# Kernel tuning notes

Measured on AMD Instinct MI355X. Metric: run time of the kernel, lower is better.

Reference implementation:

```python
import jax, jax.numpy as jnp
import numpy as np

N_NODES = 100000
N_EDGES = 3200000
F_IN = 256
CH = 16
FCN = 64


def setup_inputs() -> dict:
    key = jax.random.key(0)
    ks = jax.random.split(key, 8)
    x = jax.random.normal(ks[0], (N_NODES, F_IN), dtype=jnp.float32)
    edge_index = jax.random.randint(ks[1], (2, N_EDGES), 0, N_NODES, dtype=jnp.int64)
    edge_w = jax.random.uniform(ks[2], (N_EDGES,), dtype=jnp.float32)
    w_gcn = jax.random.normal(ks[3], (F_IN, CH), dtype=jnp.float32) * (1.0 / np.sqrt(F_IN))
    w0 = jax.random.normal(ks[4], (CH, FCN), dtype=jnp.float32) * (1.0 / np.sqrt(CH))
    b0 = jnp.zeros((FCN,), dtype=jnp.float32)
    w1 = jax.random.normal(ks[5], (FCN, 1), dtype=jnp.float32) * (1.0 / np.sqrt(FCN))
    b1 = jnp.zeros((1,), dtype=jnp.float32)
    return {"x": x, "edge_index": edge_index, "edge_w": edge_w,
            "w_gcn": w_gcn, "w0": w0, "b0": b0, "w1": w1, "b1": b1}


def reference(x, edge_index, edge_w, w_gcn, b0, b1, w0, w1):
    # GCNConv (Spektral): out = relu(A_norm @ (X @ W)); A_norm given as weighted edge list.
    # Dropout layers are identity at inference.
    src = edge_index[0]
    dst = edge_index[1]
    h = x @ w_gcn                                   # [N, CH] feature transform
    msgs = h[src] * edge_w[:, None]                 # [E, CH] gather + scale (irregular access)
    agg = jax.ops.segment_sum(msgs, dst, num_segments=N_NODES)  # [N, CH] scatter-add
    gcn_out = jax.nn.relu(agg)
    # Flatten on [N, CH] is identity (N acts as batch); per-node FCN head.
    o1 = jax.nn.relu(gcn_out @ w0 + b0)             # [N, FCN]
    o2 = o1 @ w1 + b1                               # [N, 1]
    return o2
```

## Files before the change

### kernel.cpp

```cpp
#include <hip/hip_runtime.h>

#define N_NODES 100000
#define N_EDGES 3200000
#define F_IN 256
#define CH 16
#define FCN 64

#define NPB 64
#define NBUCK 1563
#define NCHUNK 1024
#define EPB (N_EDGES / NCHUNK)
#define M (NBUCK * NCHUNK)
#define NSB (M / 1024)
#define ACCP 17
#define CAP 2560

__device__ __forceinline__ unsigned short f2bf(float f) {
    unsigned u = __float_as_uint(f);
    unsigned r = (u + 0x7FFFu + ((u >> 16) & 1u)) >> 16;
    return (unsigned short)r;
}

__global__ __launch_bounds__(256) void k_transform(const float* __restrict__ x,
                                                   const float* __restrict__ w,
                                                   unsigned short* __restrict__ h) {
    __shared__ float wlds[CH][F_IN + 4];
    int tid = threadIdx.x;
    for (int i = tid; i < F_IN * CH; i += 256) {
        int k = i >> 4, c = i & 15;
        wlds[c][k] = w[i];
    }
    __syncthreads();
    int c = tid & 15;
    int r = tid >> 4;
    int row = blockIdx.x * 16 + r;
    if (row >= N_NODES) return;
    const float4* xr = reinterpret_cast<const float4*>(x + (size_t)row * F_IN);
    const float4* wr = reinterpret_cast<const float4*>(&wlds[c][0]);
    float acc = 0.f;
    #pragma unroll 8
    for (int k4 = 0; k4 < F_IN / 4; ++k4) {
        float4 xv = xr[k4];
        float4 wv = wr[k4];
        acc = fmaf(xv.x, wv.x, acc);
        acc = fmaf(xv.y, wv.y, acc);
        acc = fmaf(xv.z, wv.z, acc);
        acc = fmaf(xv.w, wv.w, acc);
    }
    h[(size_t)row * CH + c] = f2bf(acc);
}

__global__ __launch_bounds__(256) void k_hist_rank(const int* __restrict__ ei,
                                                   unsigned short* __restrict__ rank16,
                                                   int* __restrict__ histM) {
    __shared__ int hist[NBUCK];
    int t = threadIdx.x, k = blockIdx.x;
    for (int i = t; i < NBUCK; i += 256) hist[i] = 0;
    __syncthreads();
    int base = k * EPB;
    for (int i = t; i < EPB; i += 256) {
        int e = base + i;
        int dst = ei[N_EDGES + e];
        int r = atomicAdd(&hist[dst >> 6], 1);
        rank16[e] = (unsigned short)r;
    }
    __syncthreads();
    for (int i = t; i < NBUCK; i += 256) histM[(size_t)i * NCHUNK + k] = hist[i];
}

__global__ __launch_bounds__(256) void k_scanP1(const int* __restrict__ histM,
                                                int* __restrict__ partials) {
    __shared__ int wsum[4];
    int t = threadIdx.x;
    int4 v = reinterpret_cast<const int4*>(histM)[blockIdx.x * 256 + t];
    int s = v.x + v.y + v.z + v.w;
    #pragma unroll
    for (int off = 32; off > 0; off >>= 1) s += __shfl_xor(s, off, 64);
    if ((t & 63) == 0) wsum[t >> 6] = s;
    __syncthreads();
    if (t == 0) partials[blockIdx.x] = wsum[0] + wsum[1] + wsum[2] + wsum[3];
}

__global__ __launch_bounds__(1024) void k_scanP2(const int* __restrict__ partials,
                                                 int* __restrict__ bases) {
    __shared__ int wsum[16];
    int t = threadIdx.x;
    int i0 = 2 * t, i1 = 2 * t + 1;
    int a = (i0 < NSB) ? partials[i0] : 0;
    int b = (i1 < NSB) ? partials[i1] : 0;
    int s = a + b;
    int lane = t & 63, w = t >> 6;
    int incl = s;
    #pragma unroll
    for (int off = 1; off < 64; off <<= 1) {
        int u = __shfl_up(incl, off, 64);
        if (lane >= off) incl += u;
    }
    if (lane == 63) wsum[w] = incl;
    __syncthreads();
    if (t == 0) {
        int run = 0;
        #pragma unroll
        for (int i = 0; i < 16; ++i) { int u = wsum[i]; wsum[i] = run; run += u; }
    }
    __syncthreads();
    int excl = incl - s + wsum[w];
    if (i0 <= NSB) bases[i0] = excl;
    if (i1 <= NSB) bases[i1] = excl + a;
}

__global__ __launch_bounds__(256) void k_scanP3(const int* __restrict__ histM,
                                                const int* __restrict__ bases,
                                                int* __restrict__ offs2d) {
    __shared__ int wsum[4];
    int t = threadIdx.x;
    int gi = blockIdx.x * 256 + t;
    int4 v = reinterpret_cast<const int4*>(histM)[gi];
    int s = v.x + v.y + v.z + v.w;
    int lane = t & 63, w = t >> 6;
    int incl = s;
    #pragma unroll
    for (int off = 1; off < 64; off <<= 1) {
        int u = __shfl_up(incl, off, 64);
        if (lane >= off) incl += u;
    }
    if (lane == 63) wsum[w] = incl;
    __syncthreads();
    if (t == 0) {
        int a = wsum[0], b = wsum[1], c = wsum[2];
        wsum[0] = 0; wsum[1] = a; wsum[2] = a + b; wsum[3] = a + b + c;
    }
    __syncthreads();
    int excl = incl - s + wsum[w] + bases[blockIdx.x];
    int4 o;
    o.x = excl;
    o.y = excl + v.x;
    o.z = o.y + v.y;
    o.w = o.z + v.z;
    reinterpret_cast<int4*>(offs2d)[gi] = o;
    if (blockIdx.x == 0 && t == 0) offs2d[M] = bases[NSB];
}

__global__ __launch_bounds__(256) void k_scatter2(const int* __restrict__ ei,
                                                  const float* __restrict__ ew,
                                                  const unsigned short* __restrict__ rank16,
                                                  const int* __restrict__ offs2d,
                                                  int2* __restrict__ recs) {
    __shared__ int coffs[NBUCK];
    int t = threadIdx.x, k = blockIdx.x;
    for (int i = t; i < NBUCK; i += 256) coffs[i] = offs2d[(size_t)i * NCHUNK + k];
    __syncthreads();
    int base = k * EPB;
    for (int i = t; i < EPB; i += 256) {
        int e = base + i;
        int src = ei[e];
        int dst = ei[N_EDGES + e];
        int b = dst >> 6;
        int local = dst & (NPB - 1);
        int pos = coffs[b] + (int)rank16[e];
        int2 r;
        r.x = src | (local << 17);
        r.y = __float_as_int(ew[e]);
        recs[pos] = r;
    }
}

__global__ __launch_bounds__(256) void k_agg_head(const int2* __restrict__ recs,
                                                  const int* __restrict__ offs2d,
                                                  const unsigned short* __restrict__ h,
                                                  const float* __restrict__ w0,
                                                  const float* __restrict__ b0,
                                                  const float* __restrict__ w1,
                                                  const float* __restrict__ b1,
                                                  float* __restrict__ out) {
    __shared__ int2 sorted[CAP];
    __shared__ float acc[NPB * ACCP];
    __shared__ float w0s[CH * FCN];
    __shared__ float w1s[FCN];
    __shared__ int hist64[NPB];
    __shared__ int base64[NPB];
    __shared__ int cur64[NPB];
    int t = threadIdx.x;
    int b = blockIdx.x;
    for (int i = t; i < NPB * ACCP; i += 256) acc[i] = 0.f;
    for (int i = t; i < CH * FCN; i += 256) w0s[i] = w0[i];
    if (t < FCN) w1s[t] = w1[t];
    if (t < NPB) hist64[t] = 0;
    __syncthreads();
    int start = offs2d[(size_t)b * NCHUNK];
    int end   = offs2d[(size_t)(b + 1) * NCHUNK];
    for (int j = start + t; j < end; j += 256) {
        int2 r = recs[j];
        atomicAdd(&hist64[r.x >> 17], 1);
    }
    __syncthreads();
    if (t < 64) {
        int v = hist64[t];
        int incl = v;
        #pragma unroll
        for (int off = 1; off < 64; off <<= 1) {
            int u = __shfl_up(incl, off, 64);
            if (t >= off) incl += u;
        }
        int excl = incl - v;
        base64[t] = excl;
        cur64[t] = excl;
    }
    __syncthreads();
    for (int j = start + t; j < end; j += 256) {
        int2 r = recs[j];
        int nl = r.x >> 17;
        int pos = atomicAdd(&cur64[nl], 1);
        if (pos < CAP) {
            sorted[pos] = r;
        } else {
            int src = r.x & 0x1FFFF;
            float wv = __int_as_float(r.y);
            const uint4* hp = reinterpret_cast<const uint4*>(h + (size_t)src * CH);
            uint4 ha = hp[0], hb = hp[1];
            float* a = &acc[nl * ACCP];
            unsafeAtomicAdd(a + 0,  __uint_as_float(ha.x << 16) * wv);
            unsafeAtomicAdd(a + 1,  __uint_as_float(ha.x & 0xFFFF0000u) * wv);
            unsafeAtomicAdd(a + 2,  __uint_as_float(ha.y << 16) * wv);
            unsafeAtomicAdd(a + 3,  __uint_as_float(ha.y & 0xFFFF0000u) * wv);
            unsafeAtomicAdd(a + 4,  __uint_as_float(ha.z << 16) * wv);
            unsafeAtomicAdd(a + 5,  __uint_as_float(ha.z & 0xFFFF0000u) * wv);
            unsafeAtomicAdd(a + 6,  __uint_as_float(ha.w << 16) * wv);
            unsafeAtomicAdd(a + 7,  __uint_as_float(ha.w & 0xFFFF0000u) * wv);
            unsafeAtomicAdd(a + 8,  __uint_as_float(hb.x << 16) * wv);
            unsafeAtomicAdd(a + 9,  __uint_as_float(hb.x & 0xFFFF0000u) * wv);
            unsafeAtomicAdd(a + 10, __uint_as_float(hb.y << 16) * wv);
            unsafeAtomicAdd(a + 11, __uint_as_float(hb.y & 0xFFFF0000u) * wv);
            unsafeAtomicAdd(a + 12, __uint_as_float(hb.z << 16) * wv);
            unsafeAtomicAdd(a + 13, __uint_as_float(hb.z & 0xFFFF0000u) * wv);
            unsafeAtomicAdd(a + 14, __uint_as_float(hb.w << 16) * wv);
            unsafeAtomicAdd(a + 15, __uint_as_float(hb.w & 0xFFFF0000u) * wv);
        }
    }
    __syncthreads();
    int nl = t >> 2, q = t & 3;
    int kb = base64[nl];
    int ke = min(kb + hist64[nl], CAP);
    float a0 = 0.f, a1 = 0.f, a2 = 0.f, a3 = 0.f;
    for (int k = kb; k < ke; ++k) {
        int2 r = sorted[k];
        int src  = r.x & 0x1FFFF;
        float wv = __int_as_float(r.y);
        uint2 hv = reinterpret_cast<const uint2*>(h)[src * 4 + q];
        a0 = fmaf(__uint_as_float(hv.x << 16),         wv, a0);
        a1 = fmaf(__uint_as_float(hv.x & 0xFFFF0000u), wv, a1);
        a2 = fmaf(__uint_as_float(hv.y << 16),         wv, a2);
        a3 = fmaf(__uint_as_float(hv.y & 0xFFFF0000u), wv, a3);
    }
    float* ap = &acc[nl * ACCP + q * 4];
    ap[0] += a0; ap[1] += a1; ap[2] += a2; ap[3] += a3;
    __syncthreads();
    int lane = t & 63, wv4 = t >> 6;
    float bb = b0[lane];
    float w1l = w1s[lane];
    float bias1 = b1[0];
    for (int n2 = wv4 * 16; n2 < wv4 * 16 + 16; ++n2) {
        int node = b * NPB + n2;
        if (node >= N_NODES) break;
        float o1 = bb;
        #pragma unroll
        for (int kk = 0; kk < CH; ++kk) {
            float a = fmaxf(acc[n2 * ACCP + kk], 0.f);
            o1 = fmaf(a, w0s[kk * FCN + lane], o1);
        }
        o1 = fmaxf(o1, 0.f);
        float y = o1 * w1l;
        #pragma unroll
        for (int off = 32; off > 0; off >>= 1) y += __shfl_xor(y, off, 64);
        if (lane == 0) out[node] = y + bias1;
    }
}

__global__ __launch_bounds__(256) void k_scatter_fb(const int* __restrict__ ei,
                                                    const float* __restrict__ ew,
                                                    const unsigned short* __restrict__ h,
                                                    float* __restrict__ agg) {
    long long t = (long long)blockIdx.x * 256 + threadIdx.x;
    int e = (int)(t >> 2);
    int g = (int)(t & 3);
    if (e >= N_EDGES) return;
    int src = ei[e];
    int dst = ei[N_EDGES + e];
    float w = ew[e];
    uint2 hv = reinterpret_cast<const uint2*>(h)[src * 4 + g];
    float* ap = agg + (size_t)dst * CH + g * 4;
    atomicAdd(ap + 0, __uint_as_float(hv.x << 16) * w);
    atomicAdd(ap + 1, __uint_as_float(hv.x & 0xFFFF0000u) * w);
    atomicAdd(ap + 2, __uint_as_float(hv.y << 16) * w);
    atomicAdd(ap + 3, __uint_as_float(hv.y & 0xFFFF0000u) * w);
}

__global__ __launch_bounds__(256) void k_head_fb(const float* __restrict__ agg,
                                                 const float* __restrict__ w0,
                                                 const float* __restrict__ b0,
                                                 const float* __restrict__ w1,
                                                 const float* __restrict__ b1,
                                                 float* __restrict__ out) {
    __shared__ float w0s[CH * FCN];
    __shared__ float w1s[FCN];
    int tid = threadIdx.x;
    for (int i = tid; i < CH * FCN; i += 256) w0s[i] = w0[i];
    if (tid < FCN) w1s[tid] = w1[tid];
    __syncthreads();
    int lane = tid & 63;
    int wv = tid >> 6;
    int node = blockIdx.x * 4 + wv;
    if (node >= N_NODES) return;
    const float* an = agg + (size_t)node * CH;
    float o1 = b0[lane];
    #pragma unroll
    for (int k = 0; k < CH; ++k) {
        float a = fmaxf(an[k], 0.f);
        o1 = fmaf(a, w0s[k * FCN + lane], o1);
    }
    o1 = fmaxf(o1, 0.f);
    float y = o1 * w1s[lane];
    #pragma unroll
    for (int off = 32; off > 0; off >>= 1) y += __shfl_xor(y, off, 64);
    if (lane == 0) out[node] = y + b1[0];
}

extern "C" void kernel_launch(void* const* d_in, const int* in_sizes, int n_in,
                              void* d_out, int out_size, void* d_ws, size_t ws_size,
                              hipStream_t stream) {
    const float* x  = (const float*)d_in[0];
    const int*   ei = (const int*)  d_in[1];
    const float* ew = (const float*)d_in[2];
    const float* wg = (const float*)d_in[3];
    const float* w0 = (const float*)d_in[4];
    const float* b0 = (const float*)d_in[5];
    const float* w1 = (const float*)d_in[6];
    const float* b1 = (const float*)d_in[7];
    float* out = (float*)d_out;

    char* p = (char*)d_ws;
    unsigned short* h = (unsigned short*)p;      p += 3200000;
    unsigned short* rank16 = (unsigned short*)p; p += 6400000;
    int* histM = (int*)p;                        p += (size_t)M * 4;
    int* offs2d = (int*)p;                       p += 6402304;
    int* partials = (int*)p;                     p += 6400;
    int* bases = (int*)p;                        p += 6400;
    int2* recs = (int2*)p;                       p += (size_t)N_EDGES * 8;
    const size_t need = (size_t)(p - (char*)d_ws);

    if (ws_size >= need) {
        k_transform<<<(N_NODES + 15) / 16, 256, 0, stream>>>(x, wg, h);
        k_hist_rank<<<NCHUNK, 256, 0, stream>>>(ei, rank16, histM);
        k_scanP1<<<NSB, 256, 0, stream>>>(histM, partials);
        k_scanP2<<<1, 1024, 0, stream>>>(partials, bases);
        k_scanP3<<<NSB, 256, 0, stream>>>(histM, bases, offs2d);
        k_scatter2<<<NCHUNK, 256, 0, stream>>>(ei, ew, rank16, offs2d, recs);
        k_agg_head<<<NBUCK, 256, 0, stream>>>(recs, offs2d, h, w0, b0, w1, b1, out);
    } else {
        float* agg = (float*)((char*)d_ws + 3200128);
        hipMemsetAsync(agg, 0, (size_t)N_NODES * CH * 4, stream);
        k_transform<<<(N_NODES + 15) / 16, 256, 0, stream>>>(x, wg, h);
        long long sc_threads = (long long)N_EDGES * 4;
        k_scatter_fb<<<(int)((sc_threads + 255) / 256), 256, 0, stream>>>(ei, ew, h, agg);
        k_head_fb<<<(N_NODES + 3) / 4, 256, 0, stream>>>(agg, w0, b0, w1, b1, out);
    }
}
```

Measured before the change: 403.4 us.

## Use bf16 MFMA for feature transform and flatten scatter to per-edge threads

The X@W transform now converts x and W to bf16, stages 64-row tiles in swizzled LDS and computes them with 16x16x32 bf16 MFMA instructions instead of scalar FP32 FMAs. The scatter kernel drops the per-block LDS copy of the chunk offsets and gives each thread one edge, reading its offset straight from global memory. This removes scalar FMA work and the LDS prefetch barrier. In exchange it lowers the transform's input precision to bf16 and adds scattered global reads of offs2d.

```diff
diff --git a/kernel.cpp b/kernel.cpp
--- a/kernel.cpp
+++ b/kernel.cpp
@@ -14,6 +14,10 @@
 #define NSB (M / 1024)
 #define ACCP 17
 #define CAP 2560
+#define TGRID ((N_NODES + 63) / 64)
+
+typedef __attribute__((ext_vector_type(8))) short bf16x8;
+typedef __attribute__((ext_vector_type(4))) float f32x4;
 
 __device__ __forceinline__ unsigned short f2bf(float f) {
     unsigned u = __float_as_uint(f);
@@ -24,30 +28,52 @@
 __global__ __launch_bounds__(256) void k_transform(const float* __restrict__ x,
                                                    const float* __restrict__ w,
                                                    unsigned short* __restrict__ h) {
-    __shared__ float wlds[CH][F_IN + 4];
-    int tid = threadIdx.x;
-    for (int i = tid; i < F_IN * CH; i += 256) {
-        int k = i >> 4, c = i & 15;
-        wlds[c][k] = w[i];
-    }
-    __syncthreads();
-    int c = tid & 15;
-    int r = tid >> 4;
-    int row = blockIdx.x * 16 + r;
-    if (row >= N_NODES) return;
-    const float4* xr = reinterpret_cast<const float4*>(x + (size_t)row * F_IN);
-    const float4* wr = reinterpret_cast<const float4*>(&wlds[c][0]);
-    float acc = 0.f;
-    #pragma unroll 8
-    for (int k4 = 0; k4 < F_IN / 4; ++k4) {
-        float4 xv = xr[k4];
-        float4 wv = wr[k4];
-        acc = fmaf(xv.x, wv.x, acc);
-        acc = fmaf(xv.y, wv.y, acc);
-        acc = fmaf(xv.z, wv.z, acc);
-        acc = fmaf(xv.w, wv.w, acc);
-    }
-    h[(size_t)row * CH + c] = f2bf(acc);
+    __shared__ unsigned short xs[64 * 256];
+    __shared__ unsigned short bs[8 * 64 * 8];
+    int t = threadIdx.x;
+    int r0 = blockIdx.x * 64;
+    for (int ei_ = t; ei_ < 512; ei_ += 256) {
+        int kk = ei_ >> 6, l = ei_ & 63;
+        int c = l & 15, kb = kk * 32 + ((l >> 4) << 3);
+        unsigned short tmp[8];
+        #pragma unroll
+        for (int j = 0; j < 8; ++j) tmp[j] = f2bf(w[(kb + j) * 16 + c]);
+        uint4 v;
+        v.x = tmp[0] | ((unsigned)tmp[1] << 16);
+        v.y = tmp[2] | ((unsigned)tmp[3] << 16);
+        v.z = tmp[4] | ((unsigned)tmp[5] << 16);
+        v.w = tmp[6] | ((unsigned)tmp[7] << 16);
+        *reinterpret_cast<uint4*>(&bs[ei_ * 8]) = v;
+    }
+    #pragma unroll
+    for (int i = 0; i < 16; ++i) {
+        int f = i * 256 + t;
+        int r = f >> 6, c4 = f & 63;
+        int row = r0 + r;
+        float4 xv = make_float4(0.f, 0.f, 0.f, 0.f);
+        if (row < N_NODES) xv = reinterpret_cast<const float4*>(x)[(size_t)row * 64 + c4];
+        unsigned lo = f2bf(xv.x) | ((unsigned)f2bf(xv.y) << 16);
+        unsigned hi = f2bf(xv.z) | ((unsigned)f2bf(xv.w) << 16);
+        int byte = r * 512 + ((c4 * 8) ^ ((r & 7) << 4));
+        *reinterpret_cast<uint2*>(reinterpret_cast<char*>(xs) + byte) = make_uint2(lo, hi);
+    }
+    __syncthreads();
+    int wv = t >> 6, l = t & 63;
+    int rl = (wv << 4) + (l & 15);
+    f32x4 acc = {0.f, 0.f, 0.f, 0.f};
+    #pragma unroll
+    for (int kk = 0; kk < 8; ++kk) {
+        int abyte = rl * 512 + (((kk << 6) + ((l >> 4) << 4)) ^ ((rl & 7) << 4));
+        bf16x8 av = *reinterpret_cast<const bf16x8*>(reinterpret_cast<const char*>(xs) + abyte);
+        bf16x8 bv = *reinterpret_cast<const bf16x8*>(&bs[((kk << 6) + l) * 8]);
+        acc = __builtin_amdgcn_mfma_f32_16x16x32_bf16(av, bv, acc, 0, 0, 0);
+    }
+    int col = l & 15;
+    #pragma unroll
+    for (int j = 0; j < 4; ++j) {
+        int row = r0 + (wv << 4) + ((l >> 4) << 2) + j;
+        if (row < N_NODES) h[(size_t)row * CH + col] = f2bf(acc[j]);
+    }
 }
 
 __global__ __launch_bounds__(256) void k_hist_rank(const int* __restrict__ ei,
@@ -146,23 +172,18 @@
                                                   const unsigned short* __restrict__ rank16,
                                                   const int* __restrict__ offs2d,
                                                   int2* __restrict__ recs) {
-    __shared__ int coffs[NBUCK];
-    int t = threadIdx.x, k = blockIdx.x;
-    for (int i = t; i < NBUCK; i += 256) coffs[i] = offs2d[(size_t)i * NCHUNK + k];
-    __syncthreads();
-    int base = k * EPB;
-    for (int i = t; i < EPB; i += 256) {
-        int e = base + i;
-        int src = ei[e];
-        int dst = ei[N_EDGES + e];
-        int b = dst >> 6;
-        int local = dst & (NPB - 1);
-        int pos = coffs[b] + (int)rank16[e];
-        int2 r;
-        r.x = src | (local << 17);
-        r.y = __float_as_int(ew[e]);
-        recs[pos] = r;
-    }
+    int e = blockIdx.x * 256 + threadIdx.x;
+    if (e >= N_EDGES) return;
+    int k = e / EPB;
+    int src = ei[e];
+    int dst = ei[N_EDGES + e];
+    int b = dst >> 6;
+    int local = dst & (NPB - 1);
+    int pos = offs2d[(size_t)b * NCHUNK + k] + (int)rank16[e];
+    int2 r;
+    r.x = src | (local << 17);
+    r.y = __float_as_int(ew[e]);
+    recs[pos] = r;
 }
 
 __global__ __launch_bounds__(256) void k_agg_head(const int2* __restrict__ recs,
@@ -349,17 +370,17 @@
     const size_t need = (size_t)(p - (char*)d_ws);
 
     if (ws_size >= need) {
-        k_transform<<<(N_NODES + 15) / 16, 256, 0, stream>>>(x, wg, h);
+        k_transform<<<TGRID, 256, 0, stream>>>(x, wg, h);
         k_hist_rank<<<NCHUNK, 256, 0, stream>>>(ei, rank16, histM);
         k_scanP1<<<NSB, 256, 0, stream>>>(histM, partials);
         k_scanP2<<<1, 1024, 0, stream>>>(partials, bases);
         k_scanP3<<<NSB, 256, 0, stream>>>(histM, bases, offs2d);
-        k_scatter2<<<NCHUNK, 256, 0, stream>>>(ei, ew, rank16, offs2d, recs);
+        k_scatter2<<<(N_EDGES + 255) / 256, 256, 0, stream>>>(ei, ew, rank16, offs2d, recs);
         k_agg_head<<<NBUCK, 256, 0, stream>>>(recs, offs2d, h, w0, b0, w1, b1, out);
     } else {
         float* agg = (float*)((char*)d_ws + 3200128);
         hipMemsetAsync(agg, 0, (size_t)N_NODES * CH * 4, stream);
-        k_transform<<<(N_NODES + 15) / 16, 256, 0, stream>>>(x, wg, h);
+        k_transform<<<TGRID, 256, 0, stream>>>(x, wg, h);
         long long sc_threads = (long long)N_EDGES * 4;
         k_scatter_fb<<<(int)((sc_threads + 255) / 256), 256, 0, stream>>>(ei, ew, h, agg);
         k_head_fb<<<(N_NODES + 3) / 4, 256, 0, stream>>>(agg, w0, b0, w1, b1, out);
```

New measurement: 345.4 us. 14.4% less time.
